# Optimization experiments

Measured on AMD Instinct MI355X. Metric: run time of the kernel, lower is better.

## Reference

```python
import jax, jax.numpy as jnp
import numpy as np

N = 50000
NEG_SLOPE = 0.2


def add_self_loops(edge_index, n):
    loops = jnp.arange(n, dtype=edge_index.dtype)
    return jnp.concatenate([edge_index, jnp.stack([loops, loops])], axis=1)


def gat_layer(x, edge_index, W, a_src, a_dst, b, heads, ch):
    # x: [N, F_in], W: [F_in, heads*ch], a_src/a_dst: [heads, ch], b: [heads*ch]
    n = x.shape[0]
    src, dst = edge_index[0], edge_index[1]
    h = (x @ W).reshape(n, heads, ch)                      # [N, H, C]
    alpha_src = jnp.sum(h * a_src, axis=-1)                # [N, H]
    alpha_dst = jnp.sum(h * a_dst, axis=-1)                # [N, H]
    e = jax.nn.leaky_relu(alpha_src[src] + alpha_dst[dst], NEG_SLOPE)  # [E, H]
    # segment softmax over incoming edges of each destination node
    m = jax.ops.segment_max(e, dst, num_segments=n)        # [N, H]
    ex = jnp.exp(e - m[dst])                               # [E, H]
    denom = jax.ops.segment_sum(ex, dst, num_segments=n)   # [N, H]
    alpha = ex / (denom[dst] + 1e-16)                      # [E, H]
    msg = h[src] * alpha[:, :, None]                       # [E, H, C]
    out = jax.ops.segment_sum(msg, dst, num_segments=n)    # [N, H, C]
    return out.reshape(n, heads * ch) + b


def setup_inputs() -> dict:
    key = jax.random.key(0)
    ks = jax.random.split(key, 12)
    input_dim, hidden_dim, output_dim, heads = 128, 32, 64, 4
    E = 1600000
    x = jax.random.normal(ks[0], (N, input_dim), dtype=jnp.float32)
    edge_index = jax.random.randint(ks[1], (2, E), 0, N, dtype=jnp.int64)
    s1 = 1.0 / np.sqrt(input_dim)
    s2 = 1.0 / np.sqrt(hidden_dim * heads)
    W1 = jax.random.uniform(ks[2], (input_dim, heads * hidden_dim), jnp.float32, -s1, s1)
    a_src1 = jax.random.uniform(ks[3], (heads, hidden_dim), jnp.float32, -s1, s1)
    a_dst1 = jax.random.uniform(ks[4], (heads, hidden_dim), jnp.float32, -s1, s1)
    b1 = jnp.zeros((heads * hidden_dim,), jnp.float32)
    W2 = jax.random.uniform(ks[5], (heads * hidden_dim, output_dim), jnp.float32, -s2, s2)
    a_src2 = jax.random.uniform(ks[6], (1, output_dim), jnp.float32, -s2, s2)
    a_dst2 = jax.random.uniform(ks[7], (1, output_dim), jnp.float32, -s2, s2)
    b2 = jnp.zeros((output_dim,), jnp.float32)
    return {"x": x, "edge_index": edge_index,
            "W1": W1, "a_src1": a_src1, "a_dst1": a_dst1, "b1": b1,
            "W2": W2, "a_src2": a_src2, "a_dst2": a_dst2, "b2": b2}


def reference(x, edge_index, W1, a_src1, a_dst1, b1, W2, a_src2, a_dst2, b2):
    n = x.shape[0]
    ei = add_self_loops(edge_index, n)
    h = gat_layer(x, ei, W1, a_src1, a_dst1, b1, heads=4, ch=32)
    h = jax.nn.relu(h)
    out = gat_layer(h, ei, W2, a_src2, a_dst2, b2, heads=1, ch=64)
    return out
```

## Files before the change

### kernel.cpp

```cpp
#include <hip/hip_runtime.h>
#include <hip/hip_bf16.h>
#include <hip/hip_fp16.h>


#define LRELU_SLOPE 0.2f
#define NBMAX 200
#define NBLK  512
#define BCAP  16384
#define CAPIMG 16384

typedef _Float16 f16x8 __attribute__((ext_vector_type(8)));
typedef float f32x4 __attribute__((ext_vector_type(4)));


__global__ __launch_bounds__(256) void hist_kernel(const int* __restrict__ ei_dst,
                                                   int* __restrict__ hist, int E, int chunk) {
    __shared__ int h[NBMAX];
    int t = threadIdx.x;
    for (int i = t; i < NBMAX; i += 256) h[i] = 0;
    __syncthreads();
    int begin = blockIdx.x * chunk;
    int endE = min(E, begin + chunk);
    for (int e = begin + t; e < endE; e += 256) atomicAdd(&h[ei_dst[e] >> 8], 1);
    __syncthreads();
    for (int i = t; i < NBMAX; i += 256) hist[i * NBLK + blockIdx.x] = h[i];
}

__global__ __launch_bounds__(512) void bucket_scan_kernel(int* __restrict__ hist,
                                                          int* __restrict__ gfill) {
    __shared__ int buf[2][NBLK];
    int b = blockIdx.x, t = threadIdx.x;
    buf[0][t] = hist[b * NBLK + t];
    __syncthreads();
    int pi = 0;
#pragma unroll
    for (int off = 1; off < NBLK; off <<= 1) {
        int v = buf[pi][t];
        if (t >= off) v += buf[pi][t - off];
        buf[pi ^ 1][t] = v;
        __syncthreads();
        pi ^= 1;
    }
    hist[b * NBLK + t] = (t == 0) ? 0 : buf[pi][t - 1];
    if (t == 0) gfill[b] = buf[pi][NBLK - 1];
}

__global__ __launch_bounds__(256) void scatter2_kernel(const int* __restrict__ ei_src,
                                                       const int* __restrict__ ei_dst,
                                                       const int* __restrict__ hist,
                                                       unsigned int* __restrict__ records,
                                                       int E, int chunk) {
    __shared__ int base[NBMAX];
    __shared__ int lcnt[NBMAX];
    int t = threadIdx.x;
    for (int i = t; i < NBMAX; i += 256) {
        base[i] = hist[i * NBLK + blockIdx.x];
        lcnt[i] = 0;
    }
    __syncthreads();
    int begin = blockIdx.x * chunk;
    int endE = min(E, begin + chunk);
    for (int e = begin + t; e < endE; e += 256) {
        int s = ei_src[e], d = ei_dst[e];
        int bkt = d >> 8;
        unsigned int rec = (unsigned int)d | ((unsigned int)s << 16);
        int r = atomicAdd(&lcnt[bkt], 1);
        records[(size_t)bkt * BCAP + base[bkt] + r] = rec;
    }
}

__global__ __launch_bounds__(256) void deg_kernel(const unsigned int* __restrict__ records,
                                                  const int* __restrict__ gfill,
                                                  int* __restrict__ deg, int N) {
    __shared__ int cnt[256];
    int t = threadIdx.x, b = blockIdx.x;
    cnt[t] = 1;
    __syncthreads();
    int c = gfill[b];
    const unsigned int* r = records + (size_t)b * BCAP;
    for (int i = t; i < c; i += 256) atomicAdd(&cnt[r[i] & 255], 1);
    __syncthreads();
    int gi = (b << 8) + t;
    if (gi < N) deg[gi] = cnt[t];
}

__global__ __launch_bounds__(256) void scan_blocksums_kernel(const int* __restrict__ gfill,
                                                             int* __restrict__ bsums,
                                                             int* __restrict__ row_ptr,
                                                             int nblocks, int n, int total) {
    __shared__ int buf[2][256];
    int t = threadIdx.x;
    int v0 = 0;
    if (t < nblocks) v0 = gfill[t] + min(256, n - (t << 8));
    buf[0][t] = v0;
    __syncthreads();
    int pi = 0;
#pragma unroll
    for (int off = 1; off < 256; off <<= 1) {
        int v = buf[pi][t];
        if (t >= off) v += buf[pi][t - off];
        buf[pi ^ 1][t] = v;
        __syncthreads();
        pi ^= 1;
    }
    if (t < nblocks) bsums[t] = (t == 0) ? 0 : buf[pi][t - 1];
    if (t == 0) row_ptr[n] = total;
}

__global__ __launch_bounds__(256) void scan_down_kernel(const int* __restrict__ deg,
                                                        const int* __restrict__ blockSums,
                                                        int* __restrict__ row_ptr, int n) {
    __shared__ int buf[2][256];
    int t = threadIdx.x;
    int i = blockIdx.x * 256 + t;
    int d = (i < n) ? deg[i] : 0;
    buf[0][t] = d;
    __syncthreads();
    int pi = 0;
#pragma unroll
    for (int off = 1; off < 256; off <<= 1) {
        int v = buf[pi][t];
        if (t >= off) v += buf[pi][t - off];
        buf[pi ^ 1][t] = v;
        __syncthreads();
        pi ^= 1;
    }
    if (i < n) row_ptr[i] = blockSums[blockIdx.x] + buf[pi][t] - d;
}

__global__ __launch_bounds__(256) void csr_scatter_kernel(const unsigned int* __restrict__ records,
                                                          const int* __restrict__ gfill,
                                                          const int* __restrict__ row_ptr,
                                                          unsigned short* __restrict__ col,
                                                          int N) {
    __shared__ unsigned short img[CAPIMG];
    __shared__ int lfill[256];
    int t = threadIdx.x, b = blockIdx.x;
    int bBase = b << 8;
    int bEnd = min(bBase + 256, N);
    int rbase = row_ptr[bBase];
    int size = row_ptr[bEnd] - rbase;
    bool lds = (size <= CAPIMG);
    int gi = bBase + t;
    if (gi < bEnd) {
        int rp = row_ptr[gi];
        int local = rp - rbase;
        lfill[t] = local + 1;
        if (lds) img[local] = (unsigned short)gi;
        else col[rp] = (unsigned short)gi;
    }
    __syncthreads();
    int c = gfill[b];
    const unsigned int* r = records + (size_t)b * BCAP;
    for (int i = t; i < c; i += 256) {
        unsigned int rec = r[i];
        int d8 = rec & 255;
        unsigned short s = (unsigned short)(rec >> 16);
        int p = atomicAdd(&lfill[d8], 1);
        if (lds) img[p] = s;
        else col[rbase + p] = s;
    }
    __syncthreads();
    if (lds) {
        for (int i = t; i < size; i += 256) col[rbase + i] = img[i];
    }
}


__global__ __launch_bounds__(256) void gemm1_mfma_kernel(const float* __restrict__ X,
                                                         const float* __restrict__ W,
                                                         __half* __restrict__ outh,
                                                         const float* __restrict__ a_src,
                                                         const float* __restrict__ a_dst,
                                                         float* __restrict__ as_out,
                                                         float* __restrict__ ad_out, int nrows) {
    constexpr int KP = 136;
    __shared__ _Float16 wlds[128 * KP];
    int t = threadIdx.x;
    int wv = t >> 6, lane = t & 63;
    int quad = lane >> 4, m16 = lane & 15;
    for (int i = t; i < 4096; i += 256) {
        int k = i >> 5;
        int n0 = (i & 31) << 2;
        float4 v = *(const float4*)(W + k * 128 + n0);
        wlds[(n0 + 0) * KP + k] = (_Float16)v.x;
        wlds[(n0 + 1) * KP + k] = (_Float16)v.y;
        wlds[(n0 + 2) * KP + k] = (_Float16)v.z;
        wlds[(n0 + 3) * KP + k] = (_Float16)v.w;
    }
    __syncthreads();

    int row = blockIdx.x * 64 + wv * 16 + m16;
    int rowC = min(row, nrows - 1);
    const float* xp = X + (size_t)rowC * 128;

    f32x4 acc[8];
#pragma unroll
    for (int nt = 0; nt < 8; ++nt) acc[nt] = (f32x4)0.f;

    for (int kt = 0; kt < 128; kt += 32) {
        float4 v0 = *(const float4*)(xp + kt + quad * 8);
        float4 v1 = *(const float4*)(xp + kt + quad * 8 + 4);
        f16x8 af;
        af[0] = (_Float16)v0.x; af[1] = (_Float16)v0.y;
        af[2] = (_Float16)v0.z; af[3] = (_Float16)v0.w;
        af[4] = (_Float16)v1.x; af[5] = (_Float16)v1.y;
        af[6] = (_Float16)v1.z; af[7] = (_Float16)v1.w;
#pragma unroll
        for (int nt = 0; nt < 8; ++nt) {
            f16x8 bf = *(const f16x8*)(&wlds[(nt * 16 + m16) * KP + kt + quad * 8]);
            acc[nt] = __builtin_amdgcn_mfma_f32_16x16x32_f16(af, bf, acc[nt], 0, 0, 0);
        }
    }

    float aS[8], aD[8];
#pragma unroll
    for (int nt = 0; nt < 8; ++nt) {
        aS[nt] = a_src[nt * 16 + m16];
        aD[nt] = a_dst[nt * 16 + m16];
    }
    int rowBaseW = blockIdx.x * 64 + wv * 16;
#pragma unroll
    for (int r = 0; r < 4; ++r) {
        int orow = rowBaseW + quad * 4 + r;
        bool ov = orow < nrows;
        if (ov) {
#pragma unroll
            for (int nt = 0; nt < 8; ++nt)
                outh[(size_t)orow * 128 + nt * 16 + m16] = __float2half(acc[nt][r]);
        }
#pragma unroll
        for (int h = 0; h < 4; ++h) {
            float ss = acc[2 * h][r] * aS[2 * h] + acc[2 * h + 1][r] * aS[2 * h + 1];
            float dd = acc[2 * h][r] * aD[2 * h] + acc[2 * h + 1][r] * aD[2 * h + 1];
#pragma unroll
            for (int o = 1; o < 16; o <<= 1) {
                ss += __shfl_xor(ss, o, 64);
                dd += __shfl_xor(dd, o, 64);
            }
            if (ov && m16 == h) {
                as_out[orow * 4 + h] = ss;
                ad_out[orow * 4 + h] = dd;
            }
        }
    }
}


__global__ __launch_bounds__(256) void gemm2_mfma_kernel(const __half* __restrict__ Xh,
                                                         const float* __restrict__ W,
                                                         __half* __restrict__ outh,
                                                         const float* __restrict__ a_src,
                                                         const float* __restrict__ a_dst,
                                                         float* __restrict__ as_out,
                                                         float* __restrict__ ad_out, int nrows) {
    constexpr int KP = 136;
    __shared__ _Float16 wlds[64 * KP];
    int t = threadIdx.x;
    int wv = t >> 6, lane = t & 63;
    int quad = lane >> 4, m16 = lane & 15;
    for (int i = t; i < 2048; i += 256) {
        int k = i >> 4;
        int n0 = (i & 15) << 2;
        float4 v = *(const float4*)(W + k * 64 + n0);
        wlds[(n0 + 0) * KP + k] = (_Float16)v.x;
        wlds[(n0 + 1) * KP + k] = (_Float16)v.y;
        wlds[(n0 + 2) * KP + k] = (_Float16)v.z;
        wlds[(n0 + 3) * KP + k] = (_Float16)v.w;
    }
    __syncthreads();

    int row = blockIdx.x * 64 + wv * 16 + m16;
    int rowC = min(row, nrows - 1);
    const _Float16* xp = (const _Float16*)Xh + (size_t)rowC * 128;

    f32x4 acc[4];
#pragma unroll
    for (int nt = 0; nt < 4; ++nt) acc[nt] = (f32x4)0.f;

    for (int kt = 0; kt < 128; kt += 32) {
        f16x8 af = *(const f16x8*)(xp + kt + quad * 8);
#pragma unroll
        for (int nt = 0; nt < 4; ++nt) {
            f16x8 bf = *(const f16x8*)(&wlds[(nt * 16 + m16) * KP + kt + quad * 8]);
            acc[nt] = __builtin_amdgcn_mfma_f32_16x16x32_f16(af, bf, acc[nt], 0, 0, 0);
        }
    }

    float aS[4], aD[4];
#pragma unroll
    for (int nt = 0; nt < 4; ++nt) {
        aS[nt] = a_src[nt * 16 + m16];
        aD[nt] = a_dst[nt * 16 + m16];
    }
    int rowBaseW = blockIdx.x * 64 + wv * 16;
#pragma unroll
    for (int r = 0; r < 4; ++r) {
        int orow = rowBaseW + quad * 4 + r;
        bool ov = orow < nrows;
        if (ov) {
#pragma unroll
            for (int nt = 0; nt < 4; ++nt)
                outh[(size_t)orow * 64 + nt * 16 + m16] = __float2half(acc[nt][r]);
        }
        float ss = 0.f, dd = 0.f;
#pragma unroll
        for (int nt = 0; nt < 4; ++nt) {
            ss = fmaf(acc[nt][r], aS[nt], ss);
            dd = fmaf(acc[nt][r], aD[nt], dd);
        }
#pragma unroll
        for (int o = 1; o < 16; o <<= 1) {
            ss += __shfl_xor(ss, o, 64);
            dd += __shfl_xor(dd, o, 64);
        }
        if (ov && m16 == 0) {
            as_out[orow] = ss;
            ad_out[orow] = dd;
        }
    }
}


__global__ __launch_bounds__(256) void agg1_kernel(const __half2* __restrict__ h1h,
                                                   const float* __restrict__ asrc,
                                                   const float* __restrict__ adst,
                                                   const int* __restrict__ row_ptr,
                                                   const unsigned short* __restrict__ col,
                                                   const float* __restrict__ b1,
                                                   __half2* __restrict__ out, int n) {
    int wave = threadIdx.x >> 6;
    int lane = threadIdx.x & 63;
    int node = blockIdx.x * 4 + wave;
    if (node >= n) return;
    int head = lane >> 4;
    int hp1 = lane & 3;
    int j16 = lane >> 2;
    float ad1 = adst[node * 4 + hp1];
    int start = row_ptr[node], end = row_ptr[node + 1];
    float accx = 0.f, accy = 0.f, s = 0.f;
    for (int base = start; base < end; base += 64) {
        int idx = base + lane;
        int cnt = min(64, end - base);
        int myS = (idx < end) ? (int)col[idx] : 0;
        float pr[4];
#pragma unroll
        for (int e = 0; e < 4; ++e) {
            int j = e * 16 + j16;
            int srcj = __shfl(myS, j, 64);
            float ev = asrc[srcj * 4 + hp1] + ad1;
            ev = (ev > 0.f) ? ev : LRELU_SLOPE * ev;
            pr[e] = (j < cnt) ? __expf(ev) : 0.f;
        }
#pragma unroll
        for (int e = 0; e < 4; ++e) {
            int ebase = e << 4;
            if (ebase < cnt) {
                float pre = pr[e];
                int rem4 = min(16, ((cnt - ebase) + 3) & ~3);
                for (int jj = 0; jj < rem4; jj += 4) {
                    int j0 = ebase + jj;
                    unsigned s0 = (unsigned)__shfl(myS, j0, 64);
                    unsigned s1 = (unsigned)__shfl(myS, j0 + 1, 64);
                    unsigned s2 = (unsigned)__shfl(myS, j0 + 2, 64);
                    unsigned s3 = (unsigned)__shfl(myS, j0 + 3, 64);
                    float p0 = __shfl(pre, (jj + 0) * 4 + head, 64);
                    float p1 = __shfl(pre, (jj + 1) * 4 + head, 64);
                    float p2 = __shfl(pre, (jj + 2) * 4 + head, 64);
                    float p3 = __shfl(pre, (jj + 3) * 4 + head, 64);
                    float2 f0 = __half22float2(h1h[(s0 << 6) | lane]);
                    float2 f1 = __half22float2(h1h[(s1 << 6) | lane]);
                    float2 f2 = __half22float2(h1h[(s2 << 6) | lane]);
                    float2 f3 = __half22float2(h1h[(s3 << 6) | lane]);
                    accx = fmaf(p0, f0.x, accx);
                    accy = fmaf(p0, f0.y, accy);
                    accx = fmaf(p1, f1.x, accx);
                    accy = fmaf(p1, f1.y, accy);
                    accx = fmaf(p2, f2.x, accx);
                    accy = fmaf(p2, f2.y, accy);
                    accx = fmaf(p3, f3.x, accx);
                    accy = fmaf(p3, f3.y, accy);
                    s += (p0 + p1) + (p2 + p3);
                }
            }
        }
    }
    float inv = 1.f / (s + 1e-16f);
    float2 bb = ((const float2*)b1)[lane];
    float ox = fmaxf(accx * inv + bb.x, 0.f);
    float oy = fmaxf(accy * inv + bb.y, 0.f);
    out[((unsigned)node << 6) | lane] = __floats2half2_rn(ox, oy);
}

__global__ __launch_bounds__(256) void agg2_kernel(const __half2* __restrict__ h2bh,
                                                   const float* __restrict__ asrc,
                                                   const float* __restrict__ adst,
                                                   const int* __restrict__ row_ptr,
                                                   const unsigned short* __restrict__ col,
                                                   const float* __restrict__ b2,
                                                   float* __restrict__ out, int n) {
    int wave = threadIdx.x >> 6;
    int lane = threadIdx.x & 63;
    int node = blockIdx.x * 4 + wave;
    if (node >= n) return;
    int half = lane >> 5;
    int m = lane & 31;
    float ad = adst[node];
    int start = row_ptr[node], end = row_ptr[node + 1];
    float accx = 0.f, accy = 0.f, s = 0.f;
    for (int base = start; base < end; base += 64) {
        int idx = base + lane;
        int cnt = min(64, end - base);
        int myS = (idx < end) ? (int)col[idx] : 0;
        float ev = asrc[myS] + ad;
        ev = (ev > 0.f) ? ev : LRELU_SLOPE * ev;
        float pr = (lane < cnt) ? __expf(ev) : 0.f;
        for (int j = 0; j < cnt; j += 8) {
            int j0 = j + half;
            unsigned s0 = (unsigned)__shfl(myS, j0, 64);
            unsigned s1 = (unsigned)__shfl(myS, j0 + 2, 64);
            unsigned s2 = (unsigned)__shfl(myS, j0 + 4, 64);
            unsigned s3 = (unsigned)__shfl(myS, j0 + 6, 64);
            float p0 = __shfl(pr, j0, 64);
            float p1 = __shfl(pr, j0 + 2, 64);
            float p2 = __shfl(pr, j0 + 4, 64);
            float p3 = __shfl(pr, j0 + 6, 64);
            float2 f0 = __half22float2(h2bh[(s0 << 5) | m]);
            float2 f1 = __half22float2(h2bh[(s1 << 5) | m]);
            float2 f2 = __half22float2(h2bh[(s2 << 5) | m]);
            float2 f3 = __half22float2(h2bh[(s3 << 5) | m]);
            accx = fmaf(p0, f0.x, accx);
            accy = fmaf(p0, f0.y, accy);
            accx = fmaf(p1, f1.x, accx);
            accy = fmaf(p1, f1.y, accy);
            accx = fmaf(p2, f2.x, accx);
            accy = fmaf(p2, f2.y, accy);
            accx = fmaf(p3, f3.x, accx);
            accy = fmaf(p3, f3.y, accy);
            s += (p0 + p1) + (p2 + p3);
        }
    }
    s += __shfl_xor(s, 32, 64);
    accx += __shfl_xor(accx, 32, 64);
    accy += __shfl_xor(accy, 32, 64);
    if (half == 0) {
        float inv = 1.f / (s + 1e-16f);
        float2 bb = ((const float2*)b2)[m];
        float2 o;
        o.x = accx * inv + bb.x;
        o.y = accy * inv + bb.y;
        *(float2*)(out + (size_t)node * 64 + 2 * m) = o;
    }
}


extern "C" void kernel_launch(void* const* d_in, const int* in_sizes, int n_in,
                              void* d_out, int out_size, void* d_ws, size_t ws_size,
                              hipStream_t stream) {
    const float* x      = (const float*)d_in[0];
    const int*   ei     = (const int*)d_in[1];
    const float* W1     = (const float*)d_in[2];
    const float* a_src1 = (const float*)d_in[3];
    const float* a_dst1 = (const float*)d_in[4];
    const float* b1     = (const float*)d_in[5];
    const float* W2     = (const float*)d_in[6];
    const float* a_src2 = (const float*)d_in[7];
    const float* a_dst2 = (const float*)d_in[8];
    const float* b2     = (const float*)d_in[9];
    float* out = (float*)d_out;

    const int N = in_sizes[0] / 128;
    const int E = in_sizes[1] / 2;
    const int total = E + N;
    const int nBuckets = (N + 255) >> 8;

    char* ws = (char*)d_ws;
    size_t off = 0;
    auto alloc = [&](size_t bytes) {
        void* p = ws + off;
        off += (bytes + 255) & ~(size_t)255;
        return p;
    };
    float* regionA = (float*)alloc((size_t)N * 128 * 4);
    __half* h1h   = (__half*)alloc((size_t)N * 128 * 2);
    __half* h2bh  = (__half*)alloc((size_t)N * 64 * 2);
    float* asrc1  = (float*)alloc((size_t)N * 4 * 4);
    float* adst1  = (float*)alloc((size_t)N * 4 * 4);
    float* asrc2  = (float*)alloc((size_t)N * 4);
    float* adst2  = (float*)alloc((size_t)N * 4);
    int*   deg    = (int*)alloc((size_t)N * 4);
    int*   row_ptr= (int*)alloc((size_t)(N + 1) * 4);
    int*   gfill  = (int*)alloc((size_t)nBuckets * 4);
    int*   bsums  = (int*)alloc((size_t)nBuckets * 4);
    unsigned short* col = (unsigned short*)alloc((size_t)total * 2);

    unsigned int* records = (unsigned int*)regionA;
    int* hist = (int*)(regionA + (size_t)NBMAX * BCAP);
    __half* h2in = (__half*)regionA;
    (void)ws_size; (void)n_in; (void)out_size;

    const int* ei_src = ei;
    const int* ei_dst = ei + E;

    const int chunk = (E + NBLK - 1) / NBLK;
    hist_kernel<<<NBLK, 256, 0, stream>>>(ei_dst, hist, E, chunk);
    bucket_scan_kernel<<<nBuckets, NBLK, 0, stream>>>(hist, gfill);
    scatter2_kernel<<<NBLK, 256, 0, stream>>>(ei_src, ei_dst, hist, records, E, chunk);
    deg_kernel<<<nBuckets, 256, 0, stream>>>(records, gfill, deg, N);
    scan_blocksums_kernel<<<1, 256, 0, stream>>>(gfill, bsums, row_ptr, nBuckets, N, total);
    scan_down_kernel<<<nBuckets, 256, 0, stream>>>(deg, bsums, row_ptr, N);
    csr_scatter_kernel<<<nBuckets, 256, 0, stream>>>(records, gfill, row_ptr, col, N);

    gemm1_mfma_kernel<<<(N + 63) / 64, 256, 0, stream>>>(x, W1, h1h, a_src1, a_dst1,
                                                         asrc1, adst1, N);
    agg1_kernel<<<(N + 3) / 4, 256, 0, stream>>>((const __half2*)h1h, asrc1, adst1,
                                                 row_ptr, col, b1, (__half2*)h2in, N);

    gemm2_mfma_kernel<<<(N + 63) / 64, 256, 0, stream>>>(h2in, W2, h2bh, a_src2, a_dst2,
                                                         asrc2, adst2, N);
    agg2_kernel<<<(N + 3) / 4, 256, 0, stream>>>((const __half2*)h2bh, asrc2, adst2,
                                                 row_ptr, col, b2, out, N);
}
```

Measured before the change: 254.5 us.

## Widen aggregation gathers to 8-byte f16x4 and split edges across wave halves

Both aggregation kernels now have each lane load four fp16 features (8 bytes) per edge instead of two. The wave splits into halves (agg1) or quarters (agg2) that walk different edges in parallel, with cross-lane shuffle reductions at the end. Attention logits and exps are now computed inline per gathered edge, replacing the precomputed-and-shuffled probabilities. This cuts shuffle traffic and raises bytes per memory request, but each lane recomputes the exp redundantly and the final reduction needs extra shuffles.

```diff
diff --git a/kernel.cpp b/kernel.cpp
--- a/kernel.cpp
+++ b/kernel.cpp
@@ -10,6 +10,7 @@
 #define CAPIMG 16384
 
 typedef _Float16 f16x8 __attribute__((ext_vector_type(8)));
+typedef _Float16 f16x4 __attribute__((ext_vector_type(4)));
 typedef float f32x4 __attribute__((ext_vector_type(4)));
 
 
@@ -322,77 +323,70 @@
 }
 
 
-__global__ __launch_bounds__(256) void agg1_kernel(const __half2* __restrict__ h1h,
+__global__ __launch_bounds__(256) void agg1_kernel(const __half* __restrict__ h1h,
                                                    const float* __restrict__ asrc,
                                                    const float* __restrict__ adst,
                                                    const int* __restrict__ row_ptr,
                                                    const unsigned short* __restrict__ col,
                                                    const float* __restrict__ b1,
-                                                   __half2* __restrict__ out, int n) {
+                                                   __half* __restrict__ out, int n) {
     int wave = threadIdx.x >> 6;
     int lane = threadIdx.x & 63;
     int node = blockIdx.x * 4 + wave;
     if (node >= n) return;
-    int head = lane >> 4;
-    int hp1 = lane & 3;
-    int j16 = lane >> 2;
-    float ad1 = adst[node * 4 + hp1];
+    int half = lane >> 5;
+    int m = lane & 31;
+    int head = m >> 3;
+    const f16x4* __restrict__ h4 = (const f16x4*)h1h;
+    float ad = adst[node * 4 + head];
     int start = row_ptr[node], end = row_ptr[node + 1];
-    float accx = 0.f, accy = 0.f, s = 0.f;
+    float a0c = 0.f, a1c = 0.f, a2c = 0.f, a3c = 0.f, s = 0.f;
     for (int base = start; base < end; base += 64) {
+        int cnt = min(64, end - base);
         int idx = base + lane;
-        int cnt = min(64, end - base);
         int myS = (idx < end) ? (int)col[idx] : 0;
-        float pr[4];
-#pragma unroll
-        for (int e = 0; e < 4; ++e) {
-            int j = e * 16 + j16;
-            int srcj = __shfl(myS, j, 64);
-            float ev = asrc[srcj * 4 + hp1] + ad1;
-            ev = (ev > 0.f) ? ev : LRELU_SLOPE * ev;
-            pr[e] = (j < cnt) ? __expf(ev) : 0.f;
-        }
-#pragma unroll
-        for (int e = 0; e < 4; ++e) {
-            int ebase = e << 4;
-            if (ebase < cnt) {
-                float pre = pr[e];
-                int rem4 = min(16, ((cnt - ebase) + 3) & ~3);
-                for (int jj = 0; jj < rem4; jj += 4) {
-                    int j0 = ebase + jj;
-                    unsigned s0 = (unsigned)__shfl(myS, j0, 64);
-                    unsigned s1 = (unsigned)__shfl(myS, j0 + 1, 64);
-                    unsigned s2 = (unsigned)__shfl(myS, j0 + 2, 64);
-                    unsigned s3 = (unsigned)__shfl(myS, j0 + 3, 64);
-                    float p0 = __shfl(pre, (jj + 0) * 4 + head, 64);
-                    float p1 = __shfl(pre, (jj + 1) * 4 + head, 64);
-                    float p2 = __shfl(pre, (jj + 2) * 4 + head, 64);
-                    float p3 = __shfl(pre, (jj + 3) * 4 + head, 64);
-                    float2 f0 = __half22float2(h1h[(s0 << 6) | lane]);
-                    float2 f1 = __half22float2(h1h[(s1 << 6) | lane]);
-                    float2 f2 = __half22float2(h1h[(s2 << 6) | lane]);
-                    float2 f3 = __half22float2(h1h[(s3 << 6) | lane]);
-                    accx = fmaf(p0, f0.x, accx);
-                    accy = fmaf(p0, f0.y, accy);
-                    accx = fmaf(p1, f1.x, accx);
-                    accy = fmaf(p1, f1.y, accy);
-                    accx = fmaf(p2, f2.x, accx);
-                    accy = fmaf(p2, f2.y, accy);
-                    accx = fmaf(p3, f3.x, accx);
-                    accy = fmaf(p3, f3.y, accy);
-                    s += (p0 + p1) + (p2 + p3);
-                }
-            }
-        }
-    }
-    float inv = 1.f / (s + 1e-16f);
-    float2 bb = ((const float2*)b1)[lane];
-    float ox = fmaxf(accx * inv + bb.x, 0.f);
-    float oy = fmaxf(accy * inv + bb.y, 0.f);
-    out[((unsigned)node << 6) | lane] = __floats2half2_rn(ox, oy);
-}
-
-__global__ __launch_bounds__(256) void agg2_kernel(const __half2* __restrict__ h2bh,
+        for (int j = 0; j < cnt; j += 4) {
+            int jj0 = j + half;
+            int jj1 = j + 2 + half;
+            int s0 = __shfl(myS, jj0, 64);
+            int s1 = __shfl(myS, jj1, 64);
+            f16x4 v0 = h4[s0 * 32 + m];
+            f16x4 v1 = h4[s1 * 32 + m];
+            float e0 = asrc[s0 * 4 + head] + ad;
+            float e1 = asrc[s1 * 4 + head] + ad;
+            e0 = fmaxf(e0, LRELU_SLOPE * e0);
+            e1 = fmaxf(e1, LRELU_SLOPE * e1);
+            float p0 = (jj0 < cnt) ? __expf(e0) : 0.f;
+            float p1 = (jj1 < cnt) ? __expf(e1) : 0.f;
+            a0c = fmaf(p0, (float)v0[0], a0c);
+            a1c = fmaf(p0, (float)v0[1], a1c);
+            a2c = fmaf(p0, (float)v0[2], a2c);
+            a3c = fmaf(p0, (float)v0[3], a3c);
+            a0c = fmaf(p1, (float)v1[0], a0c);
+            a1c = fmaf(p1, (float)v1[1], a1c);
+            a2c = fmaf(p1, (float)v1[2], a2c);
+            a3c = fmaf(p1, (float)v1[3], a3c);
+            s += p0 + p1;
+        }
+    }
+    a0c += __shfl_xor(a0c, 32, 64);
+    a1c += __shfl_xor(a1c, 32, 64);
+    a2c += __shfl_xor(a2c, 32, 64);
+    a3c += __shfl_xor(a3c, 32, 64);
+    s   += __shfl_xor(s, 32, 64);
+    if (half == 0) {
+        float inv = 1.f / (s + 1e-16f);
+        float4 bb = ((const float4*)b1)[m];
+        f16x4 o;
+        o[0] = (_Float16)fmaxf(fmaf(a0c, inv, bb.x), 0.f);
+        o[1] = (_Float16)fmaxf(fmaf(a1c, inv, bb.y), 0.f);
+        o[2] = (_Float16)fmaxf(fmaf(a2c, inv, bb.z), 0.f);
+        o[3] = (_Float16)fmaxf(fmaf(a3c, inv, bb.w), 0.f);
+        ((f16x4*)out)[node * 32 + m] = o;
+    }
+}
+
+__global__ __launch_bounds__(256) void agg2_kernel(const __half* __restrict__ h2bh,
                                                    const float* __restrict__ asrc,
                                                    const float* __restrict__ adst,
                                                    const int* __restrict__ row_ptr,
@@ -403,53 +397,57 @@
     int lane = threadIdx.x & 63;
     int node = blockIdx.x * 4 + wave;
     if (node >= n) return;
-    int half = lane >> 5;
-    int m = lane & 31;
+    int q = lane >> 4;
+    int m = lane & 15;
+    const f16x4* __restrict__ h4 = (const f16x4*)h2bh;
     float ad = adst[node];
     int start = row_ptr[node], end = row_ptr[node + 1];
-    float accx = 0.f, accy = 0.f, s = 0.f;
+    float a0c = 0.f, a1c = 0.f, a2c = 0.f, a3c = 0.f, s = 0.f;
     for (int base = start; base < end; base += 64) {
+        int cnt = min(64, end - base);
         int idx = base + lane;
-        int cnt = min(64, end - base);
         int myS = (idx < end) ? (int)col[idx] : 0;
-        float ev = asrc[myS] + ad;
-        ev = (ev > 0.f) ? ev : LRELU_SLOPE * ev;
-        float pr = (lane < cnt) ? __expf(ev) : 0.f;
         for (int j = 0; j < cnt; j += 8) {
-            int j0 = j + half;
-            unsigned s0 = (unsigned)__shfl(myS, j0, 64);
-            unsigned s1 = (unsigned)__shfl(myS, j0 + 2, 64);
-            unsigned s2 = (unsigned)__shfl(myS, j0 + 4, 64);
-            unsigned s3 = (unsigned)__shfl(myS, j0 + 6, 64);
-            float p0 = __shfl(pr, j0, 64);
-            float p1 = __shfl(pr, j0 + 2, 64);
-            float p2 = __shfl(pr, j0 + 4, 64);
-            float p3 = __shfl(pr, j0 + 6, 64);
-            float2 f0 = __half22float2(h2bh[(s0 << 5) | m]);
-            float2 f1 = __half22float2(h2bh[(s1 << 5) | m]);
-            float2 f2 = __half22float2(h2bh[(s2 << 5) | m]);
-            float2 f3 = __half22float2(h2bh[(s3 << 5) | m]);
-            accx = fmaf(p0, f0.x, accx);
-            accy = fmaf(p0, f0.y, accy);
-            accx = fmaf(p1, f1.x, accx);
-            accy = fmaf(p1, f1.y, accy);
-            accx = fmaf(p2, f2.x, accx);
-            accy = fmaf(p2, f2.y, accy);
-            accx = fmaf(p3, f3.x, accx);
-            accy = fmaf(p3, f3.y, accy);
-            s += (p0 + p1) + (p2 + p3);
-        }
-    }
-    s += __shfl_xor(s, 32, 64);
-    accx += __shfl_xor(accx, 32, 64);
-    accy += __shfl_xor(accy, 32, 64);
-    if (half == 0) {
+            int jj0 = j + q;
+            int jj1 = j + 4 + q;
+            int s0 = __shfl(myS, jj0, 64);
+            int s1 = __shfl(myS, jj1, 64);
+            f16x4 v0 = h4[s0 * 16 + m];
+            f16x4 v1 = h4[s1 * 16 + m];
+            float e0 = asrc[s0] + ad;
+            float e1 = asrc[s1] + ad;
+            e0 = fmaxf(e0, LRELU_SLOPE * e0);
+            e1 = fmaxf(e1, LRELU_SLOPE * e1);
+            float p0 = (jj0 < cnt) ? __expf(e0) : 0.f;
+            float p1 = (jj1 < cnt) ? __expf(e1) : 0.f;
+            a0c = fmaf(p0, (float)v0[0], a0c);
+            a1c = fmaf(p0, (float)v0[1], a1c);
+            a2c = fmaf(p0, (float)v0[2], a2c);
+            a3c = fmaf(p0, (float)v0[3], a3c);
+            a0c = fmaf(p1, (float)v1[0], a0c);
+            a1c = fmaf(p1, (float)v1[1], a1c);
+            a2c = fmaf(p1, (float)v1[2], a2c);
+            a3c = fmaf(p1, (float)v1[3], a3c);
+            s += p0 + p1;
+        }
+    }
+#pragma unroll
+    for (int o = 16; o <= 32; o <<= 1) {
+        a0c += __shfl_xor(a0c, o, 64);
+        a1c += __shfl_xor(a1c, o, 64);
+        a2c += __shfl_xor(a2c, o, 64);
+        a3c += __shfl_xor(a3c, o, 64);
+        s   += __shfl_xor(s, o, 64);
+    }
+    if (lane < 16) {
         float inv = 1.f / (s + 1e-16f);
-        float2 bb = ((const float2*)b2)[m];
-        float2 o;
-        o.x = accx * inv + bb.x;
-        o.y = accy * inv + bb.y;
-        *(float2*)(out + (size_t)node * 64 + 2 * m) = o;
+        float4 bb = ((const float4*)b2)[m];
+        float4 o;
+        o.x = fmaf(a0c, inv, bb.x);
+        o.y = fmaf(a1c, inv, bb.y);
+        o.z = fmaf(a2c, inv, bb.z);
+        o.w = fmaf(a3c, inv, bb.w);
+        ((float4*)(out + (size_t)node * 64))[m] = o;
     }
 }
 
@@ -513,11 +511,11 @@
 
     gemm1_mfma_kernel<<<(N + 63) / 64, 256, 0, stream>>>(x, W1, h1h, a_src1, a_dst1,
                                                          asrc1, adst1, N);
-    agg1_kernel<<<(N + 3) / 4, 256, 0, stream>>>((const __half2*)h1h, asrc1, adst1,
-                                                 row_ptr, col, b1, (__half2*)h2in, N);
+    agg1_kernel<<<(N + 3) / 4, 256, 0, stream>>>(h1h, asrc1, adst1,
+                                                 row_ptr, col, b1, h2in, N);
 
     gemm2_mfma_kernel<<<(N + 63) / 64, 256, 0, stream>>>(h2in, W2, h2bh, a_src2, a_dst2,
                                                          asrc2, adst2, N);
-    agg2_kernel<<<(N + 3) / 4, 256, 0, stream>>>((const __half2*)h2bh, asrc2, adst2,
+    agg2_kernel<<<(N + 3) / 4, 256, 0, stream>>>(h2bh, asrc2, adst2,
                                                  row_ptr, col, b2, out, N);
 }
```

After: 254.2 us. About the same (-0.1%).
